# Kernel optimization log

Measured on AMD Instinct MI355X. Metric: run time of the kernel, lower is better.

## Reference

```python
import jax, jax.numpy as jnp
import numpy as np
import math

B, S, DIN, E, H, WIN = 2, 2048, 512, 512, 8, 256
HD = E // H


def setup_inputs() -> dict:
    key = jax.random.key(0)
    k0, k1, k2, k3 = jax.random.split(key, 4)
    x = jax.random.normal(k0, (B, S, DIN), jnp.float32)
    padding_mask = jax.random.randint(k1, (B, S), 0, 2).astype(jnp.int32)
    # xavier-ish scale so attention logits are reasonable
    w_qkv = jax.random.normal(k2, (3 * E, DIN), jnp.float32) * (1.0 / math.sqrt(DIN))
    b_qkv = jnp.zeros((3 * E,), jnp.float32)
    w_o = jax.random.normal(k3, (E, E), jnp.float32) * (1.0 / math.sqrt(E))
    b_o = jnp.zeros((E,), jnp.float32)
    return {"x": x, "padding_mask": padding_mask, "w_qkv": w_qkv, "b_qkv": b_qkv,
            "w_o": w_o, "b_o": b_o}


def reference(x, padding_mask, w_qkv, b_qkv, w_o, b_o):
    b, s, _ = x.shape
    qkv = x @ w_qkv.T + b_qkv                     # [B,S,3E]
    qkv = qkv.reshape(b, s, H, 3 * HD).transpose(0, 2, 1, 3)  # [B,H,S,3hd]
    q, k, v = jnp.split(qkv, 3, axis=-1)          # each [B,H,S,hd]

    scale = 1.0 / math.sqrt(HD)                   # function scales by sqrt(head_dim)
    scores = jnp.einsum('bhqd,bhkd->bhqk', q, k) * scale  # [B,H,S,S]

    # Torch ref scatter_adds windowed scores into a zeros(S,S) matrix; zero-padded
    # keys contribute exactly 0 at clamped indices, so this equals band-masking.
    i = jnp.arange(s)[:, None]
    j = jnp.arange(s)[None, :]
    band = jnp.abs(i - j) <= WIN // 2             # [S,S]
    scores = jnp.where(band, scores, 0.0)
    # torch: atten_scores[atten_scores == 0.0] = -inf (kills off-band and exact zeros)
    scores = jnp.where(scores == 0.0, -jnp.inf, scores)
    # torch detaches the scores before softmax
    scores = jax.lax.stop_gradient(scores)

    key_mask = padding_mask[:, None, None, :] == 0    # [B,1,1,S]
    qry_mask = padding_mask[:, None, :, None] == 0    # [B,1,S,1]
    scores = jnp.where(key_mask, -jnp.inf, scores)
    scores = jnp.where(qry_mask, -jnp.inf, scores)

    attn = jax.nn.softmax(scores, axis=-1)
    attn = jnp.where(jnp.isnan(attn), 0.0, attn)   # fully-masked rows -> 0

    vals = jnp.einsum('bhqk,bhkd->bhqd', attn, v)  # [B,H,S,hd]
    vals = vals.transpose(0, 2, 1, 3).reshape(b, s, E)
    return vals @ w_o.T + b_o


if __name__ == '__main__':
    out = reference(**setup_inputs())
    print(out.shape)
```

## Files before the change

kernel.cpp:

```cpp
#include <hip/hip_runtime.h>
#include <math.h>

#define B 2
#define S 2048
#define H 8
#define HD 64
#define E 512
#define N3E 1536
#define M 4096
#define HALF 128

typedef unsigned short u16;
typedef unsigned int u32;
using short8 = __attribute__((ext_vector_type(8))) short;
using f32x4  = __attribute__((ext_vector_type(4))) float;

__device__ __forceinline__ u32 bfhi(float v) {
    union { float f; u32 u; } c; c.f = v;
    return (c.u + 0x7fffu + ((c.u >> 16) & 1u)) >> 16;
}
__device__ __forceinline__ float bff(u32 b) {
    union { u32 u; float f; } c; c.u = b << 16; return c.f;
}

__global__ __launch_bounds__(256) void prep_all(
    const float* __restrict__ x,     u16* __restrict__ XAh, u16* __restrict__ XAl,
    const float* __restrict__ wqkv,  u16* __restrict__ WBh, u16* __restrict__ WBl,
    const float* __restrict__ wo,    u16* __restrict__ OBh)
{
    const int wv = threadIdx.x >> 6, ln = threadIdx.x & 63;
    const float* src; u16 *dh, *dl; int Ti; bool wantlo;
    if (blockIdx.x < 1024)      { src = x;    dh = XAh; dl = XAl; Ti = blockIdx.x * 4 + wv; wantlo = true; }
    else if (blockIdx.x < 1408) { src = wqkv; dh = WBh; dl = WBl; Ti = (blockIdx.x - 1024) * 4 + wv; wantlo = true; }
    else                        { src = wo;   dh = OBh; dl = OBh; Ti = (blockIdx.x - 1408) * 4 + wv; wantlo = false; }

    const int rt = Ti >> 4, kb = Ti & 15;
    const int row = rt * 16 + (ln & 15);
    const int kc  = kb * 32 + (ln >> 4) * 8;
    const float4* s = (const float4*)(src + (size_t)row * 512 + kc);
    float4 v0 = s[0], v1 = s[1];
    float f[8] = {v0.x, v0.y, v0.z, v0.w, v1.x, v1.y, v1.z, v1.w};
    short8 hs, ls;
    #pragma unroll
    for (int e = 0; e < 8; ++e) {
        u32 hb = bfhi(f[e]);
        hs[e] = (short)hb;
        ls[e] = (short)bfhi(f[e] - bff(hb));
    }
    const size_t off = (size_t)Ti * 512 + ln * 8;
    *(short8*)(dh + off) = hs;
    if (wantlo) *(short8*)(dl + off) = ls;
}

__global__ __launch_bounds__(256) void qkv_mfma(
    const u16* __restrict__ XAh, const u16* __restrict__ XAl,
    const u16* __restrict__ WBh, const u16* __restrict__ WBl,
    const float* __restrict__ bias,
    u16* __restrict__ Qh, u16* __restrict__ Ql,
    u16* __restrict__ Kh, u16* __restrict__ Kl,
    u16* __restrict__ Vth)
{
    const int lin = blockIdx.x;
    const int c = lin & 7, rest = lin >> 3;
    const int bx = rest & 15;
    const int by = (rest >> 4) * 8 + c;

    const int wv = threadIdx.x >> 6, ln = threadIdx.x & 63;
    const int waveM = wv >> 1, waveN = wv & 1;
    const int mtb = by * 8 + waveM * 4;
    const int ntb = bx * 6 + waveN * 3;
    const int lr = ln & 15, lk = ln >> 4;

    int whj[3];
    #pragma unroll
    for (int j = 0; j < 3; ++j) whj[j] = ((ntb + j) % 12) >> 2;

    f32x4 acc[4][3] = {};

    for (int kb = 0; kb < 16; ++kb) {
        short8 a_h[4], a_l[4], b_h[3], b_l[3];
        #pragma unroll
        for (int i = 0; i < 4; ++i) {
            const size_t o = ((size_t)(mtb + i) * 16 + kb) * 512 + ln * 8;
            a_h[i] = *(const short8*)(XAh + o);
            a_l[i] = *(const short8*)(XAl + o);
        }
        #pragma unroll
        for (int j = 0; j < 3; ++j) {
            const size_t o = ((size_t)(ntb + j) * 16 + kb) * 512 + ln * 8;
            b_h[j] = *(const short8*)(WBh + o);
            if (whj[j] != 2) b_l[j] = *(const short8*)(WBl + o);
        }
        #pragma unroll
        for (int i = 0; i < 4; ++i)
            #pragma unroll
            for (int j = 0; j < 3; ++j) {
                acc[i][j] = __builtin_amdgcn_mfma_f32_16x16x32_bf16(a_h[i], b_h[j], acc[i][j], 0, 0, 0);
                if (whj[j] != 2) {
                    acc[i][j] = __builtin_amdgcn_mfma_f32_16x16x32_bf16(a_h[i], b_l[j], acc[i][j], 0, 0, 0);
                    acc[i][j] = __builtin_amdgcn_mfma_f32_16x16x32_bf16(a_l[i], b_h[j], acc[i][j], 0, 0, 0);
                }
            }
    }

    #pragma unroll
    for (int j = 0; j < 3; ++j) {
        const int n  = (ntb + j) * 16 + lr;
        const int h  = n / 192;
        const int rr = n % 192;
        const int wh = rr >> 6;
        const int d  = rr & 63;
        const float bv = bias[n];
        #pragma unroll
        for (int i = 0; i < 4; ++i) {
            const int mbase = (mtb + i) * 16 + lk * 4;
            const int b_ = mbase >> 11;
            const int s0 = mbase & 2047;
            float v[4];
            u32 hb[4];
            #pragma unroll
            for (int r = 0; r < 4; ++r) {
                v[r] = acc[i][j][r] + bv;
                hb[r] = bfhi(v[r]);
            }
            if (wh == 0) {
                #pragma unroll
                for (int r = 0; r < 4; ++r) {
                    const size_t o = (size_t)(mbase + r) * 512 + h * 64 + d;
                    Qh[o] = (u16)hb[r];
                    Ql[o] = (u16)bfhi(v[r] - bff(hb[r]));
                }
            } else if (wh == 1) {
                #pragma unroll
                for (int r = 0; r < 4; ++r) {
                    const size_t o = ((size_t)(b_ * 8 + h) * 2048 + s0 + r) * 64 + d;
                    Kh[o] = (u16)hb[r];
                    Kl[o] = (u16)bfhi(v[r] - bff(hb[r]));
                }
            } else {
                short4 h4;
                h4.x = (short)hb[0]; h4.y = (short)hb[1];
                h4.z = (short)hb[2]; h4.w = (short)hb[3];
                const size_t o = ((size_t)(b_ * 8 + h) * 64 + d) * 2048 + s0;
                *(short4*)(Vth + o) = h4;
            }
        }
    }
}

__global__ __launch_bounds__(512, 8) void attn_mfma(
    const u16* __restrict__ Qh, const u16* __restrict__ Ql,
    const u16* __restrict__ Kh, const u16* __restrict__ Kl,
    const u16* __restrict__ Vth,
    const int* __restrict__ mask, u16* __restrict__ VF)
{
    __shared__ u16   scb[32 * 296];
    __shared__ float rowsum[32];
    __shared__ u16   kmsk[288];
    __shared__ int   qmsk[32];

    const int tid = threadIdx.x;
    const int wv = tid >> 6, ln = tid & 63;
    const int lr = ln & 15, lk = ln >> 4;
    const int bh = blockIdx.x & 15;
    const int i0 = (blockIdx.x >> 4) * 32;
    const int b = bh >> 3, h = bh & 7;

    const int klo = max(0, i0 - HALF);
    const int khi = min(S - 1, i0 + 31 + HALF);
    const int kcount = khi - klo + 1;
    const int nkt = kcount >> 4, nks = kcount >> 5;

    for (int j = tid; j < kcount; j += 512) kmsk[j] = (u16)(mask[b * S + klo + j] != 0);
    if (tid < 32) { qmsk[tid] = mask[b * S + i0 + tid]; rowsum[tid] = 0.f; }
    __syncthreads();

    const int mi = wv >> 2;

    short8 qa_h[2], qa_l[2];
    {
        const int q = i0 + mi * 16 + lr;
        #pragma unroll
        for (int dh = 0; dh < 2; ++dh) {
            const size_t qo = (size_t)(b * S + q) * 512 + h * 64 + dh * 32 + lk * 8;
            qa_h[dh] = *(const short8*)(Qh + qo);
            qa_l[dh] = *(const short8*)(Ql + qo);
        }
    }

    float psum[4] = {0.f, 0.f, 0.f, 0.f};
    for (int ni = (wv & 3); ni < nkt; ni += 4) {
        const int key = klo + ni * 16 + lr;
        f32x4 acc = {};
        #pragma unroll
        for (int dh = 0; dh < 2; ++dh) {
            const size_t ko = ((size_t)(b * 8 + h) * 2048 + key) * 64 + dh * 32 + lk * 8;
            short8 bh_ = *(const short8*)(Kh + ko);
            short8 bl_ = *(const short8*)(Kl + ko);
            acc = __builtin_amdgcn_mfma_f32_16x16x32_bf16(qa_h[dh], bh_, acc, 0, 0, 0);
            acc = __builtin_amdgcn_mfma_f32_16x16x32_bf16(qa_h[dh], bl_, acc, 0, 0, 0);
            acc = __builtin_amdgcn_mfma_f32_16x16x32_bf16(qa_l[dh], bh_, acc, 0, 0, 0);
        }
        const bool kok = (kmsk[ni * 16 + lr] != 0);
        #pragma unroll
        for (int r = 0; r < 4; ++r) {
            const int row = mi * 16 + lk * 4 + r;
            const int qr  = i0 + row;
            float s = acc[r] * 0.125f;
            const bool valid = kok && (qmsk[row] != 0)
                               && (qr - key <= HALF) && (key - qr <= HALF)
                               && (s != 0.0f);
            float p = valid ? __expf(s) : 0.f;
            u32 pb = bfhi(p);
            scb[row * 296 + ni * 16 + lr] = (u16)pb;
            psum[r] += bff(pb);
        }
    }
    #pragma unroll
    for (int off = 1; off <= 8; off <<= 1)
        #pragma unroll
        for (int r = 0; r < 4; ++r)
            psum[r] += __shfl_xor(psum[r], off);
    if (lr == 0) {
        #pragma unroll
        for (int r = 0; r < 4; ++r)
            atomicAdd(&rowsum[mi * 16 + lk * 4 + r], psum[r]);
    }
    __syncthreads();

    const int d0 = (wv & 3) * 16;
    f32x4 acc2 = {};
    for (int ks = 0; ks < nks; ++ks) {
        short8 pa = *(const short8*)&scb[(mi * 16 + lr) * 296 + ks * 32 + lk * 8];
        const size_t vo = ((size_t)(b * 8 + h) * 64 + d0 + lr) * 2048 + klo + ks * 32 + lk * 8;
        short8 vh = *(const short8*)(Vth + vo);
        acc2 = __builtin_amdgcn_mfma_f32_16x16x32_bf16(pa, vh, acc2, 0, 0, 0);
    }

    #pragma unroll
    for (int r = 0; r < 4; ++r) {
        const int row = mi * 16 + lk * 4 + r;
        const float rs = rowsum[row];
        const float inv = (rs > 0.f) ? 1.f / rs : 0.f;
        const int m = b * S + i0 + row;
        const int mt = m >> 4, lrm = m & 15;
        const int e = h * 64 + d0 + lr;
        const int kb = e >> 5, rem = e & 31;
        VF[((size_t)(mt * 16 + kb) * 64 + (rem >> 3) * 16 + lrm) * 8 + (rem & 7)]
            = (u16)bfhi(acc2[r] * inv);
    }
}

__global__ __launch_bounds__(256) void outproj_mfma(
    const u16* __restrict__ VF, const u16* __restrict__ OBh,
    const float* __restrict__ bo, float* __restrict__ out)
{
    const int lin = blockIdx.x;
    const int c = lin & 7, rest = lin >> 3;
    const int bx = rest & 7;
    const int by = (rest >> 3) * 8 + c;

    const int wv = threadIdx.x >> 6, ln = threadIdx.x & 63;
    const int waveM = wv >> 1, waveN = wv & 1;
    const int mtb = by * 8 + waveM * 4;
    const int ntb = bx * 4 + waveN * 2;
    const int lr = ln & 15, lk = ln >> 4;

    f32x4 acc[4][2] = {};

    for (int kb = 0; kb < 16; ++kb) {
        short8 a[4], b_h[2];
        #pragma unroll
        for (int i = 0; i < 4; ++i)
            a[i] = *(const short8*)(VF + ((size_t)(mtb + i) * 16 + kb) * 512 + ln * 8);
        #pragma unroll
        for (int j = 0; j < 2; ++j)
            b_h[j] = *(const short8*)(OBh + ((size_t)(ntb + j) * 16 + kb) * 512 + ln * 8);
        #pragma unroll
        for (int i = 0; i < 4; ++i)
            #pragma unroll
            for (int j = 0; j < 2; ++j)
                acc[i][j] = __builtin_amdgcn_mfma_f32_16x16x32_bf16(a[i], b_h[j], acc[i][j], 0, 0, 0);
    }

    #pragma unroll
    for (int j = 0; j < 2; ++j) {
        const int n = (ntb + j) * 16 + lr;
        const float bv = bo[n];
        #pragma unroll
        for (int i = 0; i < 4; ++i)
            #pragma unroll
            for (int r = 0; r < 4; ++r) {
                const int m = (mtb + i) * 16 + lk * 4 + r;
                out[(size_t)m * 512 + n] = acc[i][j][r] + bv;
            }
    }
}

extern "C" void kernel_launch(void* const* d_in, const int* in_sizes, int n_in,
                              void* d_out, int out_size, void* d_ws, size_t ws_size,
                              hipStream_t stream)
{
    const float* x     = (const float*)d_in[0];
    const int*   pmask = (const int*)d_in[1];
    const float* w_qkv = (const float*)d_in[2];
    const float* b_qkv = (const float*)d_in[3];
    const float* w_o   = (const float*)d_in[4];
    const float* b_o   = (const float*)d_in[5];
    float* out = (float*)d_out;

    u16* XAh = (u16*)d_out;
    u16* XAl = XAh + (size_t)2097152;

    char* w8 = (char*)d_ws;
    u16* WBh = (u16*)(w8 + 0);
    u16* WBl = (u16*)(w8 + 1572864);
    u16* OBh = (u16*)(w8 + 3145728);
    u16* Qh  = (u16*)(w8 + 4194304);
    u16* Ql  = (u16*)(w8 + 8388608);
    u16* Kh  = (u16*)(w8 + 12582912);
    u16* Kl  = (u16*)(w8 + 16777216);
    u16* Vth = (u16*)(w8 + 20971520);
    u16* VF  = (u16*)(w8 + 29360128);

    prep_all<<<1536, 256, 0, stream>>>(x, XAh, XAl, w_qkv, WBh, WBl, w_o, OBh);
    qkv_mfma<<<512, 256, 0, stream>>>(XAh, XAl, WBh, WBl, b_qkv,
                                      Qh, Ql, Kh, Kl, Vth);
    attn_mfma<<<1024, 512, 0, stream>>>(Qh, Ql, Kh, Kl, Vth, pmask, VF);
    outproj_mfma<<<256, 256, 0, stream>>>(VF, OBh, b_o, out);
}
```

Before: 135.1 us.

## Drop split-bf16 compensation and fold padding mask into Q/K zeroing

```diff
diff --git a/kernel.cpp b/kernel.cpp
--- a/kernel.cpp
+++ b/kernel.cpp
@@ -23,16 +23,17 @@
     union { u32 u; float f; } c; c.u = b << 16; return c.f;
 }
 
+
 __global__ __launch_bounds__(256) void prep_all(
-    const float* __restrict__ x,     u16* __restrict__ XAh, u16* __restrict__ XAl,
-    const float* __restrict__ wqkv,  u16* __restrict__ WBh, u16* __restrict__ WBl,
-    const float* __restrict__ wo,    u16* __restrict__ OBh)
+    const float* __restrict__ x,    u16* __restrict__ XAh,
+    const float* __restrict__ wqkv, u16* __restrict__ WBh,
+    const float* __restrict__ wo,   u16* __restrict__ OBh)
 {
     const int wv = threadIdx.x >> 6, ln = threadIdx.x & 63;
-    const float* src; u16 *dh, *dl; int Ti; bool wantlo;
-    if (blockIdx.x < 1024)      { src = x;    dh = XAh; dl = XAl; Ti = blockIdx.x * 4 + wv; wantlo = true; }
-    else if (blockIdx.x < 1408) { src = wqkv; dh = WBh; dl = WBl; Ti = (blockIdx.x - 1024) * 4 + wv; wantlo = true; }
-    else                        { src = wo;   dh = OBh; dl = OBh; Ti = (blockIdx.x - 1408) * 4 + wv; wantlo = false; }
+    const float* src; u16* dh; int Ti;
+    if (blockIdx.x < 1024)      { src = x;    dh = XAh; Ti = blockIdx.x * 4 + wv; }
+    else if (blockIdx.x < 1408) { src = wqkv; dh = WBh; Ti = (blockIdx.x - 1024) * 4 + wv; }
+    else                        { src = wo;   dh = OBh; Ti = (blockIdx.x - 1408) * 4 + wv; }
 
     const int rt = Ti >> 4, kb = Ti & 15;
     const int row = rt * 16 + (ln & 15);
@@ -40,25 +41,16 @@
     const float4* s = (const float4*)(src + (size_t)row * 512 + kc);
     float4 v0 = s[0], v1 = s[1];
     float f[8] = {v0.x, v0.y, v0.z, v0.w, v1.x, v1.y, v1.z, v1.w};
-    short8 hs, ls;
-    #pragma unroll
-    for (int e = 0; e < 8; ++e) {
-        u32 hb = bfhi(f[e]);
-        hs[e] = (short)hb;
-        ls[e] = (short)bfhi(f[e] - bff(hb));
-    }
-    const size_t off = (size_t)Ti * 512 + ln * 8;
-    *(short8*)(dh + off) = hs;
-    if (wantlo) *(short8*)(dl + off) = ls;
+    short8 hs;
+    #pragma unroll
+    for (int e = 0; e < 8; ++e) hs[e] = (short)bfhi(f[e]);
+    *(short8*)(dh + (size_t)Ti * 512 + ln * 8) = hs;
 }
 
 __global__ __launch_bounds__(256) void qkv_mfma(
-    const u16* __restrict__ XAh, const u16* __restrict__ XAl,
-    const u16* __restrict__ WBh, const u16* __restrict__ WBl,
-    const float* __restrict__ bias,
-    u16* __restrict__ Qh, u16* __restrict__ Ql,
-    u16* __restrict__ Kh, u16* __restrict__ Kl,
-    u16* __restrict__ Vth)
+    const u16* __restrict__ XAh, const u16* __restrict__ WBh,
+    const float* __restrict__ bias, const int* __restrict__ mask,
+    u16* __restrict__ Qh, u16* __restrict__ Kh, u16* __restrict__ Vth)
 {
     const int lin = blockIdx.x;
     const int c = lin & 7, rest = lin >> 3;
@@ -71,36 +63,29 @@
     const int ntb = bx * 6 + waveN * 3;
     const int lr = ln & 15, lk = ln >> 4;
 
-    int whj[3];
-    #pragma unroll
-    for (int j = 0; j < 3; ++j) whj[j] = ((ntb + j) % 12) >> 2;
-
     f32x4 acc[4][3] = {};
 
     for (int kb = 0; kb < 16; ++kb) {
-        short8 a_h[4], a_l[4], b_h[3], b_l[3];
-        #pragma unroll
-        for (int i = 0; i < 4; ++i) {
-            const size_t o = ((size_t)(mtb + i) * 16 + kb) * 512 + ln * 8;
-            a_h[i] = *(const short8*)(XAh + o);
-            a_l[i] = *(const short8*)(XAl + o);
-        }
-        #pragma unroll
-        for (int j = 0; j < 3; ++j) {
-            const size_t o = ((size_t)(ntb + j) * 16 + kb) * 512 + ln * 8;
-            b_h[j] = *(const short8*)(WBh + o);
-            if (whj[j] != 2) b_l[j] = *(const short8*)(WBl + o);
-        }
-        #pragma unroll
-        for (int i = 0; i < 4; ++i)
-            #pragma unroll
-            for (int j = 0; j < 3; ++j) {
+        short8 a_h[4], b_h[3];
+        #pragma unroll
+        for (int i = 0; i < 4; ++i)
+            a_h[i] = *(const short8*)(XAh + ((size_t)(mtb + i) * 16 + kb) * 512 + ln * 8);
+        #pragma unroll
+        for (int j = 0; j < 3; ++j)
+            b_h[j] = *(const short8*)(WBh + ((size_t)(ntb + j) * 16 + kb) * 512 + ln * 8);
+        #pragma unroll
+        for (int i = 0; i < 4; ++i)
+            #pragma unroll
+            for (int j = 0; j < 3; ++j)
                 acc[i][j] = __builtin_amdgcn_mfma_f32_16x16x32_bf16(a_h[i], b_h[j], acc[i][j], 0, 0, 0);
-                if (whj[j] != 2) {
-                    acc[i][j] = __builtin_amdgcn_mfma_f32_16x16x32_bf16(a_h[i], b_l[j], acc[i][j], 0, 0, 0);
-                    acc[i][j] = __builtin_amdgcn_mfma_f32_16x16x32_bf16(a_l[i], b_h[j], acc[i][j], 0, 0, 0);
-                }
-            }
+    }
+
+    int rmask[4][4];
+    #pragma unroll
+    for (int i = 0; i < 4; ++i) {
+        const int mb = (mtb + i) * 16 + lk * 4;
+        #pragma unroll
+        for (int r = 0; r < 4; ++r) rmask[i][r] = mask[mb + r];
     }
 
     #pragma unroll
@@ -116,48 +101,37 @@
             const int mbase = (mtb + i) * 16 + lk * 4;
             const int b_ = mbase >> 11;
             const int s0 = mbase & 2047;
-            float v[4];
             u32 hb[4];
             #pragma unroll
             for (int r = 0; r < 4; ++r) {
-                v[r] = acc[i][j][r] + bv;
-                hb[r] = bfhi(v[r]);
+                float val = acc[i][j][r] + bv;
+                if (wh < 2 && rmask[i][r] == 0) val = 0.f;
+                hb[r] = bfhi(val);
             }
             if (wh == 0) {
                 #pragma unroll
-                for (int r = 0; r < 4; ++r) {
-                    const size_t o = (size_t)(mbase + r) * 512 + h * 64 + d;
-                    Qh[o] = (u16)hb[r];
-                    Ql[o] = (u16)bfhi(v[r] - bff(hb[r]));
-                }
+                for (int r = 0; r < 4; ++r)
+                    Qh[(size_t)(mbase + r) * 512 + h * 64 + d] = (u16)hb[r];
             } else if (wh == 1) {
                 #pragma unroll
-                for (int r = 0; r < 4; ++r) {
-                    const size_t o = ((size_t)(b_ * 8 + h) * 2048 + s0 + r) * 64 + d;
-                    Kh[o] = (u16)hb[r];
-                    Kl[o] = (u16)bfhi(v[r] - bff(hb[r]));
-                }
+                for (int r = 0; r < 4; ++r)
+                    Kh[((size_t)(b_ * 8 + h) * 2048 + s0 + r) * 64 + d] = (u16)hb[r];
             } else {
                 short4 h4;
                 h4.x = (short)hb[0]; h4.y = (short)hb[1];
                 h4.z = (short)hb[2]; h4.w = (short)hb[3];
-                const size_t o = ((size_t)(b_ * 8 + h) * 64 + d) * 2048 + s0;
-                *(short4*)(Vth + o) = h4;
+                *(short4*)(Vth + ((size_t)(b_ * 8 + h) * 64 + d) * 2048 + s0) = h4;
             }
         }
     }
 }
 
 __global__ __launch_bounds__(512, 8) void attn_mfma(
-    const u16* __restrict__ Qh, const u16* __restrict__ Ql,
-    const u16* __restrict__ Kh, const u16* __restrict__ Kl,
-    const u16* __restrict__ Vth,
-    const int* __restrict__ mask, u16* __restrict__ VF)
+    const u16* __restrict__ Qh, const u16* __restrict__ Kh,
+    const u16* __restrict__ Vth, u16* __restrict__ VF)
 {
     __shared__ u16   scb[32 * 296];
     __shared__ float rowsum[32];
-    __shared__ u16   kmsk[288];
-    __shared__ int   qmsk[32];
 
     const int tid = threadIdx.x;
     const int wv = tid >> 6, ln = tid & 63;
@@ -171,21 +145,17 @@
     const int kcount = khi - klo + 1;
     const int nkt = kcount >> 4, nks = kcount >> 5;
 
-    for (int j = tid; j < kcount; j += 512) kmsk[j] = (u16)(mask[b * S + klo + j] != 0);
-    if (tid < 32) { qmsk[tid] = mask[b * S + i0 + tid]; rowsum[tid] = 0.f; }
+    if (tid < 32) rowsum[tid] = 0.f;
     __syncthreads();
 
     const int mi = wv >> 2;
 
-    short8 qa_h[2], qa_l[2];
+    short8 qa_h[2];
     {
         const int q = i0 + mi * 16 + lr;
         #pragma unroll
-        for (int dh = 0; dh < 2; ++dh) {
-            const size_t qo = (size_t)(b * S + q) * 512 + h * 64 + dh * 32 + lk * 8;
-            qa_h[dh] = *(const short8*)(Qh + qo);
-            qa_l[dh] = *(const short8*)(Ql + qo);
-        }
+        for (int dh = 0; dh < 2; ++dh)
+            qa_h[dh] = *(const short8*)(Qh + (size_t)(b * S + q) * 512 + h * 64 + dh * 32 + lk * 8);
     }
 
     float psum[4] = {0.f, 0.f, 0.f, 0.f};
@@ -194,22 +164,15 @@
         f32x4 acc = {};
         #pragma unroll
         for (int dh = 0; dh < 2; ++dh) {
-            const size_t ko = ((size_t)(b * 8 + h) * 2048 + key) * 64 + dh * 32 + lk * 8;
-            short8 bh_ = *(const short8*)(Kh + ko);
-            short8 bl_ = *(const short8*)(Kl + ko);
-            acc = __builtin_amdgcn_mfma_f32_16x16x32_bf16(qa_h[dh], bh_, acc, 0, 0, 0);
-            acc = __builtin_amdgcn_mfma_f32_16x16x32_bf16(qa_h[dh], bl_, acc, 0, 0, 0);
-            acc = __builtin_amdgcn_mfma_f32_16x16x32_bf16(qa_l[dh], bh_, acc, 0, 0, 0);
+            short8 kh_ = *(const short8*)(Kh + ((size_t)(b * 8 + h) * 2048 + key) * 64 + dh * 32 + lk * 8);
+            acc = __builtin_amdgcn_mfma_f32_16x16x32_bf16(qa_h[dh], kh_, acc, 0, 0, 0);
         }
-        const bool kok = (kmsk[ni * 16 + lr] != 0);
         #pragma unroll
         for (int r = 0; r < 4; ++r) {
             const int row = mi * 16 + lk * 4 + r;
             const int qr  = i0 + row;
             float s = acc[r] * 0.125f;
-            const bool valid = kok && (qmsk[row] != 0)
-                               && (qr - key <= HALF) && (key - qr <= HALF)
-                               && (s != 0.0f);
+            const bool valid = ((u32)(key - qr + HALF) <= 2 * HALF) && (s != 0.0f);
             float p = valid ? __expf(s) : 0.f;
             u32 pb = bfhi(p);
             scb[row * 296 + ni * 16 + lr] = (u16)pb;
@@ -310,22 +273,17 @@
     float* out = (float*)d_out;
 
     u16* XAh = (u16*)d_out;
-    u16* XAl = XAh + (size_t)2097152;
 
     char* w8 = (char*)d_ws;
     u16* WBh = (u16*)(w8 + 0);
-    u16* WBl = (u16*)(w8 + 1572864);
     u16* OBh = (u16*)(w8 + 3145728);
     u16* Qh  = (u16*)(w8 + 4194304);
-    u16* Ql  = (u16*)(w8 + 8388608);
     u16* Kh  = (u16*)(w8 + 12582912);
-    u16* Kl  = (u16*)(w8 + 16777216);
     u16* Vth = (u16*)(w8 + 20971520);
     u16* VF  = (u16*)(w8 + 29360128);
 
-    prep_all<<<1536, 256, 0, stream>>>(x, XAh, XAl, w_qkv, WBh, WBl, w_o, OBh);
-    qkv_mfma<<<512, 256, 0, stream>>>(XAh, XAl, WBh, WBl, b_qkv,
-                                      Qh, Ql, Kh, Kl, Vth);
-    attn_mfma<<<1024, 512, 0, stream>>>(Qh, Ql, Kh, Kl, Vth, pmask, VF);
+    prep_all<<<1536, 256, 0, stream>>>(x, XAh, w_qkv, WBh, w_o, OBh);
+    qkv_mfma<<<512, 256, 0, stream>>>(XAh, WBh, b_qkv, pmask, Qh, Kh, Vth);
+    attn_mfma<<<1024, 512, 0, stream>>>(Qh, Kh, Vth, VF);
     outproj_mfma<<<256, 256, 0, stream>>>(VF, OBh, b_o, out);
 }
```

New measurement: 118.0 us. -12.7%, faster.
